# Optimization experiments

Hardware: AMD Instinct MI355X
Metric: run time of the kernel (lower is better)

Reference implementation:

```python
import jax, jax.numpy as jnp
import numpy as np

V, E, T_MAX, H, L = 20000, 384, 512, 8, 8
D = E // H  # head size 48
FF = 4 * E


def setup_inputs() -> dict:
    key = jax.random.key(0)
    ks = jax.random.split(key, 24)
    B, T = 16, 512
    s = 0.02
    return {
        "index": jax.random.randint(ks[0], (B, T), 0, V, dtype=jnp.int64),
        "targets": jax.random.randint(ks[1], (B, T), 0, V, dtype=jnp.int64),
        "tok_emb": s * jax.random.normal(ks[2], (V, E), jnp.float32),
        "pos_emb": s * jax.random.normal(ks[3], (T_MAX, E), jnp.float32),
        "Wq": s * jax.random.normal(ks[4], (L, E, H, D), jnp.float32),
        "bq": jnp.zeros((L, H, D), jnp.float32),
        "Wk": s * jax.random.normal(ks[5], (L, E, H, D), jnp.float32),
        "bk": jnp.zeros((L, H, D), jnp.float32),
        "Wv": s * jax.random.normal(ks[6], (L, E, H, D), jnp.float32),
        "bv": jnp.zeros((L, H, D), jnp.float32),
        "Wo": s * jax.random.normal(ks[7], (L, E, E), jnp.float32),
        "bo": jnp.zeros((L, E), jnp.float32),
        "ln1_g": jnp.ones((L, E), jnp.float32),
        "ln1_b": jnp.zeros((L, E), jnp.float32),
        "ln2_g": jnp.ones((L, E), jnp.float32),
        "ln2_b": jnp.zeros((L, E), jnp.float32),
        "W1": s * jax.random.normal(ks[8], (L, E, FF), jnp.float32),
        "b1": jnp.zeros((L, FF), jnp.float32),
        "W2": s * jax.random.normal(ks[9], (L, FF, E), jnp.float32),
        "b2": jnp.zeros((L, E), jnp.float32),
        "lnf_g": jnp.ones((E,), jnp.float32),
        "lnf_b": jnp.zeros((E,), jnp.float32),
        "lm_b": jnp.zeros((V,), jnp.float32),
    }


def layernorm(x, g, b, eps=1e-5):
    mu = jnp.mean(x, axis=-1, keepdims=True)
    var = jnp.var(x, axis=-1, keepdims=True)
    return (x - mu) * jax.lax.rsqrt(var + eps) * g + b


def reference(index, targets, tok_emb, pos_emb, Wq, bq, Wk, bk, Wv, bv, Wo, bo,
              ln1_g, ln1_b, ln2_g, ln2_b, W1, b1, W2, b2, lnf_g, lnf_b, lm_b):
    B, T = index.shape
    x = tok_emb[index] + pos_emb[:T]  # [B,T,E]
    causal = jnp.tril(jnp.ones((T, T), bool))
    scale = D ** -0.5
    for l in range(L):
        h = layernorm(x, ln1_g[l], ln1_b[l])
        q = jnp.einsum('bte,ehd->bthd', h, Wq[l]) + bq[l]
        k = jnp.einsum('bte,ehd->bthd', h, Wk[l]) + bk[l]
        v = jnp.einsum('bte,ehd->bthd', h, Wv[l]) + bv[l]
        scores = jnp.einsum('bqhd,bkhd->bhqk', q, k) * scale
        scores = jnp.where(causal, scores, -jnp.inf)
        w = jax.nn.softmax(scores, axis=-1)
        attn = jnp.einsum('bhqk,bkhd->bqhd', w, v).reshape(B, T, E)
        x = x + attn @ Wo[l] + bo[l]
        h2 = layernorm(x, ln2_g[l], ln2_b[l])
        ff = jax.nn.gelu(h2 @ W1[l] + b1[l], approximate=False) @ W2[l] + b2[l]
        x = x + ff
    x = layernorm(x, lnf_g, lnf_b)
    logits = x @ tok_emb.T + lm_b  # tied weights
    logits = logits.reshape(B * T, V)
    logp = jax.nn.log_softmax(logits, axis=-1)
    loss = -jnp.mean(jnp.take_along_axis(logp, targets.reshape(-1, 1), axis=-1))
    return logits, loss
```

## Files before the change

### kernel.cpp

```cpp
#include <hip/hip_runtime.h>
#include <hip/hip_bf16.h>
#include <math.h>

#define M_ROWS 8192
#define E_DIM 384
#define FF_DIM 1536
#define V_DIM 20000
#define VPAD 20096
#define N_LAYER 8
#define QK_SCALE 0.14433756729740643f
#define PSTRIDE 320

typedef __bf16 bf16x8 __attribute__((ext_vector_type(8)));
typedef short  s16x8  __attribute__((ext_vector_type(8)));
typedef float  f32x4  __attribute__((ext_vector_type(4)));
typedef __hip_bfloat16 bf16_t;

__device__ __forceinline__ void gl2lds16(const void* g, void* l) {
    __builtin_amdgcn_global_load_lds((const __attribute__((address_space(1))) void*)g,
                                     (__attribute__((address_space(3))) void*)l, 16, 0, 0);
}
__device__ __forceinline__ unsigned short bf16bits(float v) {
    return __builtin_bit_cast(unsigned short, __float2bfloat16(v));
}

__global__ __launch_bounds__(256) void tconv_kernel(
    const float* __restrict__ in, bf16_t* __restrict__ out,
    int K, int N, int outRows, int rowoff)
{
    __shared__ float tile[32][33];
    const int n0 = blockIdx.x * 32, k0 = blockIdx.y * 32;
    const float* ip = in + (size_t)blockIdx.z * K * N;
    bf16_t* op = out + (size_t)blockIdx.z * outRows * K;
    const int tx = threadIdx.x & 31, ty = threadIdx.x >> 5;
#pragma unroll
    for (int i = 0; i < 32; i += 8)
        tile[ty + i][tx] = ip[(size_t)(k0 + ty + i) * N + n0 + tx];
    __syncthreads();
#pragma unroll
    for (int i = 0; i < 32; i += 8)
        op[(size_t)(rowoff + n0 + ty + i) * K + k0 + tx] = __float2bfloat16(tile[tx][ty + i]);
}

__global__ __launch_bounds__(256) void tokconv_kernel(
    const float* __restrict__ tok, bf16_t* __restrict__ out)
{
    const size_t total = (size_t)VPAD * E_DIM;
    for (size_t i = blockIdx.x * 256ull + threadIdx.x; i < total; i += gridDim.x * 256ull) {
        int row = (int)(i / E_DIM);
        int col = (int)(i - (size_t)row * E_DIM);
        float v = (row < V_DIM) ? tok[(size_t)row * E_DIM + col] : 0.f;
        out[i] = __float2bfloat16(v);
    }
}

__global__ __launch_bounds__(256) void bqkv_kernel(
    const float* __restrict__ bq, const float* __restrict__ bk,
    const float* __restrict__ bv, float* __restrict__ o)
{
    int i = blockIdx.x * 256 + threadIdx.x;
    if (i < N_LAYER * 1152) {
        int l = i / 1152, c = i - l * 1152;
        float v = (c < 384) ? bq[l * 384 + c] : (c < 768) ? bk[l * 384 + c - 384] : bv[l * 384 + c - 768];
        o[i] = v;
    }
}

__global__ __launch_bounds__(256) void embed_kernel(
    const int* __restrict__ idx, const float* __restrict__ tok,
    const float* __restrict__ pos, float* __restrict__ x)
{
    int row = blockIdx.x * 4 + (threadIdx.x >> 6);
    int lane = threadIdx.x & 63;
    int t = row & 511;
    int id = idx[row];
    const float* tr = tok + (size_t)id * E_DIM;
    const float* pr = pos + (size_t)t * E_DIM;
    float* xr = x + (size_t)row * E_DIM;
#pragma unroll
    for (int i = 0; i < 6; i++) { int c = lane + i * 64; xr[c] = tr[c] + pr[c]; }
}

__global__ __launch_bounds__(256) void ln_kernel(
    const float* __restrict__ x, const float* __restrict__ g,
    const float* __restrict__ b, bf16_t* __restrict__ out)
{
    int row = blockIdx.x * 4 + (threadIdx.x >> 6);
    int lane = threadIdx.x & 63;
    const float* xr = x + (size_t)row * E_DIM;
    float vals[6];
    float s = 0.f;
#pragma unroll
    for (int i = 0; i < 6; i++) { vals[i] = xr[lane + i * 64]; s += vals[i]; }
#pragma unroll
    for (int off = 1; off < 64; off <<= 1) s += __shfl_xor(s, off);
    float mu = s * (1.f / E_DIM);
    float sq = 0.f;
#pragma unroll
    for (int i = 0; i < 6; i++) { float d = vals[i] - mu; sq += d * d; }
#pragma unroll
    for (int off = 1; off < 64; off <<= 1) sq += __shfl_xor(sq, off);
    float rstd = rsqrtf(sq * (1.f / E_DIM) + 1e-5f);
    bf16_t* orow = out + (size_t)row * E_DIM;
#pragma unroll
    for (int i = 0; i < 6; i++) {
        int c = lane + i * 64;
        orow[c] = __float2bfloat16((vals[i] - mu) * rstd * g[c] + b[c]);
    }
}

template <int MODE, int MREP, bool SWAP>
__global__ __launch_bounds__(256) void gemm_kernel(
    const bf16_t* __restrict__ A, const bf16_t* __restrict__ Bt,
    const float* __restrict__ bias, void* __restrict__ Cv, void* __restrict__ C2,
    int Ncols, int K)
{
    constexpr int BMR = MREP * 32;
    __shared__ __align__(16) short smem[8192];
    const int t = threadIdx.x;
    const int w = t >> 6, lane = t & 63;
    const int wm = w >> 1, wn = w & 1;
    const int bm = (MODE == 3 ? blockIdx.x : blockIdx.y) * BMR;
    const int bn = (MODE == 3 ? blockIdx.y : blockIdx.x) * 128;

    f32x4 acc[MREP][4];
#pragma unroll
    for (int m = 0; m < MREP; m++)
#pragma unroll
        for (int n = 0; n < 4; n++)
            acc[m][n] = (f32x4){0.f, 0.f, 0.f, 0.f};

    const int lg = lane >> 4;
    const int ll = lane & 15;

    for (int kt = 0; kt < K; kt += 32) {
        __syncthreads();
#pragma unroll
        for (int i = 0; i < MREP / 2; i++) {
            int li = i * 256 + t;
            int g = li >> (MREP == 4 ? 7 : 6);
            int row = li & (BMR - 1);
            gl2lds16(A + (size_t)(bm + row) * K + kt + g * 8,
                     smem + (size_t)(i * 256 + w * 64) * 8);
        }
#pragma unroll
        for (int i = 0; i < 2; i++) {
            int li = i * 256 + t;
            gl2lds16(Bt + (size_t)(bn + (li & 127)) * K + kt + (li >> 7) * 8,
                     smem + 4096 + (size_t)(i * 256 + w * 64) * 8);
        }
        asm volatile("s_waitcnt vmcnt(0)" ::: "memory");
        __syncthreads();

        bf16x8 af[MREP], bfr[4];
#pragma unroll
        for (int m = 0; m < MREP; m++)
            af[m] = __builtin_bit_cast(bf16x8,
                *(const s16x8*)&smem[(lg * BMR + wm * (BMR / 2) + m * 16 + ll) * 8]);
#pragma unroll
        for (int n = 0; n < 4; n++)
            bfr[n] = __builtin_bit_cast(bf16x8,
                *(const s16x8*)&smem[4096 + (lg * 128 + wn * 64 + n * 16 + ll) * 8]);
#pragma unroll
        for (int m = 0; m < MREP; m++)
#pragma unroll
            for (int n = 0; n < 4; n++) {
                if (SWAP)
                    acc[m][n] = __builtin_amdgcn_mfma_f32_16x16x32_bf16(bfr[n], af[m], acc[m][n], 0, 0, 0);
                else
                    acc[m][n] = __builtin_amdgcn_mfma_f32_16x16x32_bf16(af[m], bfr[n], acc[m][n], 0, 0, 0);
            }
    }

    if constexpr (SWAP) {
        const int rowm0 = bm + wm * (BMR / 2) + ll;
        const int coln0 = bn + wn * 64 + lg * 4;

        if constexpr (MODE == 4) {
            bf16_t* qkvb = (bf16_t*)Cv;
            const float sc = (bn >= 384) ? 1.f : QK_SCALE;
#pragma unroll
            for (int n = 0; n < 4; n++) {
                const int coln = coln0 + n * 16;
                const float4 b4 = *(const float4*)&bias[coln];
#pragma unroll
                for (int m = 0; m < MREP; m++) {
                    const int row = rowm0 + m * 16;
                    ushort4 pk;
                    pk.x = bf16bits((acc[m][n][0] + b4.x) * sc);
                    pk.y = bf16bits((acc[m][n][1] + b4.y) * sc);
                    pk.z = bf16bits((acc[m][n][2] + b4.z) * sc);
                    pk.w = bf16bits((acc[m][n][3] + b4.w) * sc);
                    *(ushort4*)&qkvb[(size_t)row * 1152 + coln] = pk;
                }
            }
        } else if constexpr (MODE == 1) {
            float* C = (float*)Cv;
#pragma unroll
            for (int n = 0; n < 4; n++) {
                const int coln = coln0 + n * 16;
                const float4 b4 = *(const float4*)&bias[coln];
#pragma unroll
                for (int m = 0; m < MREP; m++) {
                    const int row = rowm0 + m * 16;
                    float4 cv = *(float4*)&C[(size_t)row * Ncols + coln];
                    cv.x += acc[m][n][0] + b4.x;
                    cv.y += acc[m][n][1] + b4.y;
                    cv.z += acc[m][n][2] + b4.z;
                    cv.w += acc[m][n][3] + b4.w;
                    *(float4*)&C[(size_t)row * Ncols + coln] = cv;
                }
            }
        } else if constexpr (MODE == 2) {
            bf16_t* O = (bf16_t*)Cv;
#pragma unroll
            for (int n = 0; n < 4; n++) {
                const int coln = coln0 + n * 16;
                const float4 b4 = *(const float4*)&bias[coln];
#pragma unroll
                for (int m = 0; m < MREP; m++) {
                    const int row = rowm0 + m * 16;
                    float v0 = acc[m][n][0] + b4.x, v1 = acc[m][n][1] + b4.y;
                    float v2 = acc[m][n][2] + b4.z, v3 = acc[m][n][3] + b4.w;
                    v0 = 0.5f * v0 * (1.f + erff(v0 * 0.70710678118654752f));
                    v1 = 0.5f * v1 * (1.f + erff(v1 * 0.70710678118654752f));
                    v2 = 0.5f * v2 * (1.f + erff(v2 * 0.70710678118654752f));
                    v3 = 0.5f * v3 * (1.f + erff(v3 * 0.70710678118654752f));
                    ushort4 pk;
                    pk.x = bf16bits(v0); pk.y = bf16bits(v1);
                    pk.z = bf16bits(v2); pk.w = bf16bits(v3);
                    *(ushort4*)&O[(size_t)row * Ncols + coln] = pk;
                }
            }
        } else if constexpr (MODE == 3) {
            float* C = (float*)Cv;
            float* pbuf = (float*)C2;
            const int ptile = blockIdx.y * 2 + wn;
#pragma unroll
            for (int m = 0; m < MREP; m++) {
                const int row = rowm0 + m * 16;
                float se = 0.f;
#pragma unroll
                for (int n = 0; n < 4; n++) {
                    const int coln = coln0 + n * 16;
                    if (coln + 3 < Ncols) {
                        const float4 b4 = *(const float4*)&bias[coln];
                        float4 v;
                        v.x = acc[m][n][0] + b4.x;
                        v.y = acc[m][n][1] + b4.y;
                        v.z = acc[m][n][2] + b4.z;
                        v.w = acc[m][n][3] + b4.w;
                        *(float4*)&C[(size_t)row * Ncols + coln] = v;
                        se += __expf(v.x) + __expf(v.y) + __expf(v.z) + __expf(v.w);
                    } else {
#pragma unroll
                        for (int e = 0; e < 4; e++) {
                            int col = coln + e;
                            if (col < Ncols) {
                                float v = acc[m][n][e] + bias[col];
                                C[(size_t)row * Ncols + col] = v;
                                se += __expf(v);
                            }
                        }
                    }
                }
                se += __shfl_xor(se, 16);
                se += __shfl_xor(se, 32);
                if (lg == 0) pbuf[(size_t)row * PSTRIDE + ptile] = se;
            }
        }
        return;
    }

    {
        const int r0 = bm + wm * (BMR / 2) + lg * 4;
        const int c0 = bn + wn * 64 + ll;
        bf16_t* vtb = (bf16_t*)C2;
#pragma unroll
        for (int n = 0; n < 4; n++) {
            const int col = c0 + n * 16;
            const float bv = bias[col];
            const int hh = col / 48, dd = col - hh * 48;
#pragma unroll
            for (int m = 0; m < MREP; m++) {
                const int row0 = r0 + m * 16;
                const int bb = row0 >> 9, tt2 = row0 & 511;
                ushort4 pk;
                pk.x = bf16bits(acc[m][n][0] + bv);
                pk.y = bf16bits(acc[m][n][1] + bv);
                pk.z = bf16bits(acc[m][n][2] + bv);
                pk.w = bf16bits(acc[m][n][3] + bv);
                *(ushort4*)&vtb[((size_t)(bb * 8 + hh) * 48 + dd) * 512 + tt2] = pk;
            }
        }
    }
}

__global__ __launch_bounds__(256) void attn_kernel(
    const bf16_t* __restrict__ qkvb, const bf16_t* __restrict__ vt,
    bf16_t* __restrict__ o)
{
    const int qt = blockIdx.x, bh = blockIdx.y;
    const int b = bh >> 3, h = bh & 7;
    __shared__ unsigned short psm[4608];
    const int tid = threadIdx.x;
    const int w = tid >> 6, lane = tid & 63;
    const int ll = lane & 15, g = lane >> 4;
    const int q0 = qt * 64;
    const int q_abs = q0 + ll * 4 + w;

    const bf16_t* qrow = qkvb + (size_t)(b * 512 + q_abs) * 1152 + h * 48;
    bf16x8 qf0 = __builtin_bit_cast(bf16x8, *(const s16x8*)(qrow + g * 8));
    bf16x8 qf1 = {};
    if (g < 2) qf1 = __builtin_bit_cast(bf16x8, *(const s16x8*)(qrow + 32 + g * 8));

    f32x4 oacc[3];
#pragma unroll
    for (int df = 0; df < 3; df++) oacc[df] = (f32x4){0.f, 0.f, 0.f, 0.f};
    float mrun = -1e30f, ssum = 0.f;

    const bf16_t* kb0 = qkvb + (size_t)b * 512 * 1152 + 384 + h * 48;
    const bf16_t* vb0 = vt + (size_t)bh * 48 * 512;
    const int ntiles = 2 * (qt + 1);

    for (int kt = 0; kt < ntiles; kt++) {
        const int kbase = kt * 32;
        f32x4 sfr[2];
#pragma unroll
        for (int f = 0; f < 2; f++) {
            const bf16_t* krow = kb0 + (size_t)(kbase + f * 16 + ll) * 1152;
            bf16x8 k0 = __builtin_bit_cast(bf16x8, *(const s16x8*)(krow + g * 8));
            bf16x8 k1 = {};
            if (g < 2) k1 = __builtin_bit_cast(bf16x8, *(const s16x8*)(krow + 32 + g * 8));
            f32x4 z = {0.f, 0.f, 0.f, 0.f};
            z = __builtin_amdgcn_mfma_f32_16x16x32_bf16(k0, qf0, z, 0, 0, 0);
            z = __builtin_amdgcn_mfma_f32_16x16x32_bf16(k1, qf1, z, 0, 0, 0);
            sfr[f] = z;
        }
        bf16x8 vf[3];
#pragma unroll
        for (int df = 0; df < 3; df++)
            vf[df] = __builtin_bit_cast(bf16x8,
                *(const s16x8*)(vb0 + (size_t)(df * 16 + ll) * 512 + kbase + g * 8));

        float p[8];
        float tmax = -1e30f;
#pragma unroll
        for (int f = 0; f < 2; f++)
#pragma unroll
            for (int j = 0; j < 4; j++) {
                int key = kbase + f * 16 + g * 4 + j;
                float sv = sfr[f][j];
                sv = (key > q_abs) ? -1e30f : sv;
                p[f * 4 + j] = sv;
                tmax = fmaxf(tmax, sv);
            }
        tmax = fmaxf(tmax, __shfl_xor(tmax, 16));
        tmax = fmaxf(tmax, __shfl_xor(tmax, 32));
        float mnew = fmaxf(mrun, tmax);
        float corr = __expf(mrun - mnew);
        float psum = 0.f;
#pragma unroll
        for (int i = 0; i < 8; i++) { p[i] = __expf(p[i] - mnew); psum += p[i]; }
        psum += __shfl_xor(psum, 16);
        psum += __shfl_xor(psum, 32);
        ssum = ssum * corr + psum;
        mrun = mnew;
#pragma unroll
        for (int df = 0; df < 3; df++)
#pragma unroll
            for (int j = 0; j < 4; j++) oacc[df][j] *= corr;

        const int pbase = (w * 2 + (kt & 1)) * 576;
#pragma unroll
        for (int f = 0; f < 2; f++)
#pragma unroll
            for (int j = 0; j < 4; j++)
                psm[pbase + (f * 16 + g * 4 + j) * 18 + ll] =
                    __builtin_bit_cast(unsigned short, __float2bfloat16(p[f * 4 + j]));
        s16x8 pr;
#pragma unroll
        for (int i = 0; i < 8; i++)
            pr[i] = (short)psm[pbase + (g * 8 + i) * 18 + ll];
        bf16x8 pf = __builtin_bit_cast(bf16x8, pr);
#pragma unroll
        for (int df = 0; df < 3; df++)
            oacc[df] = __builtin_amdgcn_mfma_f32_16x16x32_bf16(vf[df], pf, oacc[df], 0, 0, 0);
    }

    float inv = 1.f / ssum;
    bf16_t* orow = o + (size_t)(b * 512 + q_abs) * 384 + h * 48;
#pragma unroll
    for (int df = 0; df < 3; df++) {
        ushort4 pk;
        pk.x = bf16bits(oacc[df][0] * inv);
        pk.y = bf16bits(oacc[df][1] * inv);
        pk.z = bf16bits(oacc[df][2] * inv);
        pk.w = bf16bits(oacc[df][3] * inv);
        *(ushort4*)&orow[df * 16 + g * 4] = pk;
    }
}

__global__ __launch_bounds__(256) void loss_row2_kernel(
    const float* __restrict__ pbuf, const float* __restrict__ logits,
    const int* __restrict__ targets, float* __restrict__ rowloss)
{
    int row = blockIdx.x * 4 + (threadIdx.x >> 6);
    int lane = threadIdx.x & 63;
    const float* pr = pbuf + (size_t)row * PSTRIDE;
    float s = 0.f;
    for (int i = lane; i < 314; i += 64) s += pr[i];
#pragma unroll
    for (int off = 1; off < 64; off <<= 1) s += __shfl_xor(s, off);
    if (lane == 0) {
        int tgt = targets[row];
        rowloss[row] = logf(s) - logits[(size_t)row * V_DIM + tgt];
    }
}

__global__ __launch_bounds__(256) void loss_reduce_kernel(
    const float* __restrict__ rowloss, float* __restrict__ out)
{
    int t = threadIdx.x;
    __shared__ float red[4];
    float s = 0.f;
    for (int i = t; i < M_ROWS; i += 256) s += rowloss[i];
#pragma unroll
    for (int off = 1; off < 64; off <<= 1) s += __shfl_xor(s, off);
    if ((t & 63) == 0) red[t >> 6] = s;
    __syncthreads();
    if (t == 0) out[0] = (red[0] + red[1] + red[2] + red[3]) * (1.f / M_ROWS);
}

extern "C" void kernel_launch(void* const* d_in, const int* in_sizes, int n_in,
                              void* d_out, int out_size, void* d_ws, size_t ws_size,
                              hipStream_t stream)
{
    const int*   index   = (const int*)d_in[0];
    const int*   targets = (const int*)d_in[1];
    const float* tok_emb = (const float*)d_in[2];
    const float* pos_emb = (const float*)d_in[3];
    const float* Wq = (const float*)d_in[4];
    const float* bq = (const float*)d_in[5];
    const float* Wk = (const float*)d_in[6];
    const float* bk = (const float*)d_in[7];
    const float* Wv = (const float*)d_in[8];
    const float* bv = (const float*)d_in[9];
    const float* Wo = (const float*)d_in[10];
    const float* bo = (const float*)d_in[11];
    const float* ln1_g = (const float*)d_in[12];
    const float* ln1_b = (const float*)d_in[13];
    const float* ln2_g = (const float*)d_in[14];
    const float* ln2_b = (const float*)d_in[15];
    const float* W1 = (const float*)d_in[16];
    const float* b1 = (const float*)d_in[17];
    const float* W2 = (const float*)d_in[18];
    const float* b2 = (const float*)d_in[19];
    const float* lnf_g = (const float*)d_in[20];
    const float* lnf_b = (const float*)d_in[21];
    const float* lm_b  = (const float*)d_in[22];

    float* out = (float*)d_out;
    char* wsb = (char*)d_ws;

    float*  x     = (float*)(wsb + 0);
    bf16_t* hbuf  = (bf16_t*)(wsb + 12582912);
    bf16_t* obuf  = (bf16_t*)(wsb + 18874368);
    bf16_t* qkvb  = (bf16_t*)(wsb + 25165824);
    bf16_t* vtb   = (bf16_t*)(wsb + 44040192);
    bf16_t* ffmid = (bf16_t*)(wsb + 18874368);
    bf16_t* tokb  = (bf16_t*)(wsb + 50331648);
    bf16_t* qkvw  = (bf16_t*)(wsb + 65765376);
    bf16_t* wo_t  = (bf16_t*)(wsb + 72843264);
    bf16_t* w1_t  = (bf16_t*)(wsb + 75202560);
    bf16_t* w2_t  = (bf16_t*)(wsb + 84639744);
    float*  bqkv  = (float*)(wsb + 94076928);
    float*  rowloss = (float*)(wsb + 94113792);
    float*  pbuf  = (float*)(wsb + 94146560);

    tokconv_kernel<<<2048, 256, 0, stream>>>(tok_emb, tokb);
    tconv_kernel<<<dim3(12, 12, 8), 256, 0, stream>>>(Wq, qkvw, 384, 384, 1152, 0);
    tconv_kernel<<<dim3(12, 12, 8), 256, 0, stream>>>(Wk, qkvw, 384, 384, 1152, 384);
    tconv_kernel<<<dim3(12, 12, 8), 256, 0, stream>>>(Wv, qkvw, 384, 384, 1152, 768);
    tconv_kernel<<<dim3(12, 12, 8), 256, 0, stream>>>(Wo, wo_t, 384, 384, 384, 0);
    tconv_kernel<<<dim3(48, 12, 8), 256, 0, stream>>>(W1, w1_t, 384, 1536, 1536, 0);
    tconv_kernel<<<dim3(12, 48, 8), 256, 0, stream>>>(W2, w2_t, 1536, 384, 384, 0);
    bqkv_kernel<<<36, 256, 0, stream>>>(bq, bk, bv, bqkv);

    embed_kernel<<<2048, 256, 0, stream>>>(index, tok_emb, pos_emb, x);

    for (int l = 0; l < N_LAYER; l++) {
        const bf16_t* qkvw_l = qkvw + (size_t)l * 1152 * 384;
        const float*  bqkv_l = bqkv + l * 1152;
        ln_kernel<<<2048, 256, 0, stream>>>(x, ln1_g + l * E_DIM, ln1_b + l * E_DIM, hbuf);
        gemm_kernel<4, 4, true><<<dim3(6, 64), 256, 0, stream>>>(
            hbuf, qkvw_l, bqkv_l, qkvb, nullptr, 1152, 384);
        gemm_kernel<5, 4, false><<<dim3(3, 64), 256, 0, stream>>>(
            hbuf, qkvw_l + (size_t)768 * 384, bqkv_l + 768, nullptr, vtb, 384, 384);
        attn_kernel<<<dim3(8, 128), 256, 0, stream>>>(qkvb, vtb, obuf);
        gemm_kernel<1, 2, true><<<dim3(3, 128), 256, 0, stream>>>(
            obuf, wo_t + (size_t)l * 384 * 384, bo + l * E_DIM, x, nullptr, 384, 384);
        ln_kernel<<<2048, 256, 0, stream>>>(x, ln2_g + l * E_DIM, ln2_b + l * E_DIM, hbuf);
        gemm_kernel<2, 4, true><<<dim3(12, 64), 256, 0, stream>>>(
            hbuf, w1_t + (size_t)l * 1536 * 384, b1 + l * FF_DIM, ffmid, nullptr, 1536, 384);
        gemm_kernel<1, 2, true><<<dim3(3, 128), 256, 0, stream>>>(
            ffmid, w2_t + (size_t)l * 384 * 1536, b2 + l * E_DIM, x, nullptr, 384, 1536);
    }

    ln_kernel<<<2048, 256, 0, stream>>>(x, lnf_g, lnf_b, hbuf);
    gemm_kernel<3, 4, true><<<dim3(64, 157), 256, 0, stream>>>(
        hbuf, tokb, lm_b, out, pbuf, V_DIM, 384);

    loss_row2_kernel<<<2048, 256, 0, stream>>>(pbuf, out, targets, rowloss);
    loss_reduce_kernel<<<1, 256, 0, stream>>>(rowloss, out + (size_t)M_ROWS * V_DIM);
}
```

Measured before the change: 1.995 ms.

## Prefetch K tiles in attention, shrink LM-head tile, size LDS by tile

The attention kernel now software-pipelines its K-fragment loads, fetching the next key tile while computing the current one with a two-tile unrolled loop. The GEMM's shared memory is sized from BMR, so the MREP=2 variants use less LDS and can fit more blocks per CU. The LM-head GEMM switches from 128-row to 64-row tiles (twice as many blocks, MODE 3 writes more partial columns per row?), and pbuf moves into the reused qkv workspace region. This adds register pressure in attention and may change the partial-sum layout for the loss.

Result: slower. 2.052 ms (+2.9%).

```diff
diff --git a/kernel.cpp b/kernel.cpp
--- a/kernel.cpp
+++ b/kernel.cpp
@@ -10,6 +10,7 @@
 #define N_LAYER 8
 #define QK_SCALE 0.14433756729740643f
 #define PSTRIDE 320
+#define NPART 314
 
 typedef __bf16 bf16x8 __attribute__((ext_vector_type(8)));
 typedef short  s16x8  __attribute__((ext_vector_type(8)));
@@ -116,7 +117,7 @@
     int Ncols, int K)
 {
     constexpr int BMR = MREP * 32;
-    __shared__ __align__(16) short smem[8192];
+    __shared__ __align__(16) short smem[4096 + BMR * 32];
     const int t = threadIdx.x;
     const int w = t >> 6, lane = t & 63;
     const int wm = w >> 1, wn = w & 1;
@@ -147,7 +148,7 @@
         for (int i = 0; i < 2; i++) {
             int li = i * 256 + t;
             gl2lds16(Bt + (size_t)(bn + (li & 127)) * K + kt + (li >> 7) * 8,
-                     smem + 4096 + (size_t)(i * 256 + w * 64) * 8);
+                     smem + BMR * 32 + (size_t)(i * 256 + w * 64) * 8);
         }
         asm volatile("s_waitcnt vmcnt(0)" ::: "memory");
         __syncthreads();
@@ -160,7 +161,7 @@
 #pragma unroll
         for (int n = 0; n < 4; n++)
             bfr[n] = __builtin_bit_cast(bf16x8,
-                *(const s16x8*)&smem[4096 + (lg * 128 + wn * 64 + n * 16 + ll) * 8]);
+                *(const s16x8*)&smem[BMR * 32 + (lg * 128 + wn * 64 + n * 16 + ll) * 8]);
 #pragma unroll
         for (int m = 0; m < MREP; m++)
 #pragma unroll
@@ -319,29 +320,42 @@
     for (int df = 0; df < 3; df++) oacc[df] = (f32x4){0.f, 0.f, 0.f, 0.f};
     float mrun = -1e30f, ssum = 0.f;
 
-    const bf16_t* kb0 = qkvb + (size_t)b * 512 * 1152 + 384 + h * 48;
-    const bf16_t* vb0 = vt + (size_t)bh * 48 * 512;
+    const bf16_t* kptr = qkvb + (size_t)b * 512 * 1152 + 384 + h * 48;
+    const bf16_t* vptr = vt + (size_t)bh * 48 * 512;
     const int ntiles = 2 * (qt + 1);
 
-    for (int kt = 0; kt < ntiles; kt++) {
-        const int kbase = kt * 32;
-        f32x4 sfr[2];
-#pragma unroll
-        for (int f = 0; f < 2; f++) {
-            const bf16_t* krow = kb0 + (size_t)(kbase + f * 16 + ll) * 1152;
-            bf16x8 k0 = __builtin_bit_cast(bf16x8, *(const s16x8*)(krow + g * 8));
-            bf16x8 k1 = {};
-            if (g < 2) k1 = __builtin_bit_cast(bf16x8, *(const s16x8*)(krow + 32 + g * 8));
-            f32x4 z = {0.f, 0.f, 0.f, 0.f};
-            z = __builtin_amdgcn_mfma_f32_16x16x32_bf16(k0, qf0, z, 0, 0, 0);
-            z = __builtin_amdgcn_mfma_f32_16x16x32_bf16(k1, qf1, z, 0, 0, 0);
-            sfr[f] = z;
-        }
+    auto loadK = [&](int kbase, bf16x8& c00, bf16x8& c01, bf16x8& c10, bf16x8& c11) {
+        const bf16_t* kr0 = kptr + (size_t)(kbase + ll) * 1152;
+        const bf16_t* kr1 = kptr + (size_t)(kbase + 16 + ll) * 1152;
+        c00 = __builtin_bit_cast(bf16x8, *(const s16x8*)(kr0 + g * 8));
+        c10 = __builtin_bit_cast(bf16x8, *(const s16x8*)(kr1 + g * 8));
+        bf16x8 z = {};
+        c01 = (g < 2) ? __builtin_bit_cast(bf16x8, *(const s16x8*)(kr0 + 32 + g * 8)) : z;
+        c11 = (g < 2) ? __builtin_bit_cast(bf16x8, *(const s16x8*)(kr1 + 32 + g * 8)) : z;
+    };
+
+    auto doTile = [&](int kbase, int parity,
+                      const bf16x8& c00, const bf16x8& c01, const bf16x8& c10, const bf16x8& c11,
+                      bool pf, int nbase,
+                      bf16x8& n00, bf16x8& n01, bf16x8& n10, bf16x8& n11) {
         bf16x8 vf[3];
 #pragma unroll
         for (int df = 0; df < 3; df++)
             vf[df] = __builtin_bit_cast(bf16x8,
-                *(const s16x8*)(vb0 + (size_t)(df * 16 + ll) * 512 + kbase + g * 8));
+                *(const s16x8*)(vptr + (size_t)(df * 16 + ll) * 512 + kbase + g * 8));
+        if (pf) loadK(nbase, n00, n01, n10, n11);
+
+        f32x4 sfr[2];
+        {
+            f32x4 z0 = {0.f, 0.f, 0.f, 0.f};
+            z0 = __builtin_amdgcn_mfma_f32_16x16x32_bf16(c00, qf0, z0, 0, 0, 0);
+            z0 = __builtin_amdgcn_mfma_f32_16x16x32_bf16(c01, qf1, z0, 0, 0, 0);
+            sfr[0] = z0;
+            f32x4 z1 = {0.f, 0.f, 0.f, 0.f};
+            z1 = __builtin_amdgcn_mfma_f32_16x16x32_bf16(c10, qf0, z1, 0, 0, 0);
+            z1 = __builtin_amdgcn_mfma_f32_16x16x32_bf16(c11, qf1, z1, 0, 0, 0);
+            sfr[1] = z1;
+        }
 
         float p[8];
         float tmax = -1e30f;
@@ -371,21 +385,29 @@
 #pragma unroll
             for (int j = 0; j < 4; j++) oacc[df][j] *= corr;
 
-        const int pbase = (w * 2 + (kt & 1)) * 576;
+        const int pbase = (w * 2 + parity) * 576;
 #pragma unroll
         for (int f = 0; f < 2; f++)
 #pragma unroll
             for (int j = 0; j < 4; j++)
-                psm[pbase + (f * 16 + g * 4 + j) * 18 + ll] =
-                    __builtin_bit_cast(unsigned short, __float2bfloat16(p[f * 4 + j]));
+                psm[pbase + (f * 16 + g * 4 + j) * 18 + ll] = bf16bits(p[f * 4 + j]);
         s16x8 pr;
 #pragma unroll
         for (int i = 0; i < 8; i++)
             pr[i] = (short)psm[pbase + (g * 8 + i) * 18 + ll];
-        bf16x8 pf = __builtin_bit_cast(bf16x8, pr);
+        bf16x8 pfr = __builtin_bit_cast(bf16x8, pr);
 #pragma unroll
         for (int df = 0; df < 3; df++)
-            oacc[df] = __builtin_amdgcn_mfma_f32_16x16x32_bf16(vf[df], pf, oacc[df], 0, 0, 0);
+            oacc[df] = __builtin_amdgcn_mfma_f32_16x16x32_bf16(vf[df], pfr, oacc[df], 0, 0, 0);
+    };
+
+    bf16x8 kA0, kA1, kA2, kA3, kB0, kB1, kB2, kB3;
+    loadK(0, kA0, kA1, kA2, kA3);
+    for (int kt = 0; kt < ntiles; kt += 2) {
+        doTile(kt * 32, 0, kA0, kA1, kA2, kA3,
+               true, (kt + 1) * 32, kB0, kB1, kB2, kB3);
+        doTile((kt + 1) * 32, 1, kB0, kB1, kB2, kB3,
+               (kt + 2) < ntiles, (kt + 2) * 32, kA0, kA1, kA2, kA3);
     }
 
     float inv = 1.f / ssum;
@@ -409,7 +431,7 @@
     int lane = threadIdx.x & 63;
     const float* pr = pbuf + (size_t)row * PSTRIDE;
     float s = 0.f;
-    for (int i = lane; i < 314; i += 64) s += pr[i];
+    for (int i = lane; i < NPART; i += 64) s += pr[i];
 #pragma unroll
     for (int off = 1; off < 64; off <<= 1) s += __shfl_xor(s, off);
     if (lane == 0) {
@@ -469,6 +491,7 @@
     bf16_t* qkvb  = (bf16_t*)(wsb + 25165824);
     bf16_t* vtb   = (bf16_t*)(wsb + 44040192);
     bf16_t* ffmid = (bf16_t*)(wsb + 18874368);
+    float*  pbuf  = (float*)(wsb + 25165824);
     bf16_t* tokb  = (bf16_t*)(wsb + 50331648);
     bf16_t* qkvw  = (bf16_t*)(wsb + 65765376);
     bf16_t* wo_t  = (bf16_t*)(wsb + 72843264);
@@ -476,7 +499,6 @@
     bf16_t* w2_t  = (bf16_t*)(wsb + 84639744);
     float*  bqkv  = (float*)(wsb + 94076928);
     float*  rowloss = (float*)(wsb + 94113792);
-    float*  pbuf  = (float*)(wsb + 94146560);
 
     tokconv_kernel<<<2048, 256, 0, stream>>>(tok_emb, tokb);
     tconv_kernel<<<dim3(12, 12, 8), 256, 0, stream>>>(Wq, qkvw, 384, 384, 1152, 0);
@@ -508,7 +530,7 @@
     }
 
     ln_kernel<<<2048, 256, 0, stream>>>(x, lnf_g, lnf_b, hbuf);
-    gemm_kernel<3, 4, true><<<dim3(64, 157), 256, 0, stream>>>(
+    gemm_kernel<3, 2, true><<<dim3(128, 157), 256, 0, stream>>>(
         hbuf, tokb, lm_b, out, pbuf, V_DIM, 384);
 
     loss_row2_kernel<<<2048, 256, 0, stream>>>(pbuf, out, targets, rowloss);
```
